# Optimization experiments

Hardware: AMD Instinct MI355X
Metric: run time of the kernel (lower is better)

## Reference

```python
import math
import jax, jax.numpy as jnp
import numpy as np

CLUSTER_RATIO1 = 0.0625
CLUSTER_RATIO2 = 0.35
K_LAYER1 = 8
K_LAYER2 = 3


def _dpc_knn(x, cluster_num, k, key):
    """Density-peak clustering with KNN density. x: [B,N,C] -> idx_cluster [B,N]."""
    B, N, C = x.shape
    sq = jnp.sum(x * x, axis=-1)  # [B,N]
    d2 = sq[:, :, None] + sq[:, None, :] - 2.0 * jnp.einsum('bnc,bmc->bnm', x, x)
    dist = jnp.sqrt(jnp.maximum(d2, 0.0)) / jnp.sqrt(jnp.asarray(C, x.dtype))  # cdist / C**0.5
    # k nearest (smallest) distances
    neg_dn, _ = jax.lax.top_k(-dist, k)
    dist_nearest = -neg_dn  # [B,N,k]
    density = jnp.exp(-jnp.mean(dist_nearest ** 2, axis=-1))
    density = density + jax.random.uniform(key, density.shape, dtype=density.dtype) * 1e-6
    mask = (density[:, None, :] > density[:, :, None]).astype(x.dtype)  # [B,N,N]
    dist_max = jnp.max(dist.reshape(B, -1), axis=-1)[:, None, None]
    parent_dist = jnp.min(dist * mask + dist_max * (1.0 - mask), axis=-1)  # [B,N]
    score = parent_dist * density
    _, index_down = jax.lax.top_k(score, cluster_num)  # [B,cluster_num] cluster centers
    # assign each token to nearest center
    dm = jnp.take_along_axis(dist, index_down[:, :, None], axis=1)  # [B,cluster_num,N]
    idx_cluster = jnp.argmin(dm, axis=1)  # [B,N]
    bidx = jnp.arange(B)[:, None]
    idx_cluster = idx_cluster.at[bidx, index_down].set(
        jnp.broadcast_to(jnp.arange(cluster_num)[None, :], index_down.shape))
    return idx_cluster


def _merge_tokens(x, idx_cluster, cluster_num):
    """Weighted (uniform) scatter-mean of tokens into clusters. x: [B,N,C]."""
    B, N, C = x.shape
    flat = (idx_cluster + jnp.arange(B)[:, None] * cluster_num).reshape(-1)  # [B*N]
    ones = jnp.ones((B * N,), x.dtype)
    all_w = jax.ops.segment_sum(ones, flat, num_segments=B * cluster_num) + 1e-6
    norm_w = 1.0 / all_w[flat]  # token_weight == 1
    merged = jax.ops.segment_sum(x.reshape(B * N, C) * norm_w[:, None], flat,
                                 num_segments=B * cluster_num)
    return merged.reshape(B, cluster_num, C)


def _group(meta1, meta2, idx_cluster2, score_w, score_b):
    """Reorder [meta2[v]; members of cluster v from meta1] per cluster, scaled by modulation."""
    T, K1, C = meta1.shape
    K2 = meta2.shape[1]
    modu = jax.nn.softmax(meta2.mean(axis=2) @ score_w.T + score_b, axis=-1)  # [T,K2]
    # composite sort key: (cluster_id, 0 for meta2 center, 1+i for meta1 member i) -> stable grouping
    cid = jnp.concatenate([jnp.broadcast_to(jnp.arange(K2)[None, :], (T, K2)),
                           idx_cluster2], axis=1)  # [T,K2+K1]
    pos = jnp.concatenate([jnp.zeros((T, K2), jnp.int32),
                           jnp.broadcast_to(jnp.arange(1, K1 + 1, dtype=jnp.int32)[None, :], (T, K1))],
                          axis=1)
    sort_key = cid * (K1 + 2) + pos
    order = jnp.argsort(sort_key, axis=1)  # stable; keys are unique anyway
    tokens = jnp.concatenate([meta2, meta1], axis=1)  # [T,K2+K1,C]
    sorted_tokens = jnp.take_along_axis(tokens, order[:, :, None], axis=1)
    sorted_cid = jnp.take_along_axis(cid, order, axis=1)
    scale = jnp.take_along_axis(modu, sorted_cid, axis=1)  # [T,K2+K1]
    return sorted_tokens * scale[:, :, None]


def setup_inputs() -> dict:
    key = jax.random.key(0)
    k1, k2, k3 = jax.random.split(key, 3)
    T, N, C = 128, 256, 1408
    vis_embed = jax.random.normal(k1, (T, N, C), dtype=jnp.float32)
    score_w = jax.random.normal(k2, (6, 6), dtype=jnp.float32) * 0.1
    score_b = jax.random.normal(k3, (6,), dtype=jnp.float32) * 0.1
    return {"vis_embed": vis_embed, "score_w": score_w, "score_b": score_b}


def reference(vis_embed, score_w, score_b):
    T, N, C = vis_embed.shape
    cn1 = max(math.ceil(N * CLUSTER_RATIO1), 1)      # 16
    cn2 = max(math.ceil(cn1 * CLUSTER_RATIO2), 1)    # 6
    nk = jax.random.split(jax.random.key(42), 2)
    idx1 = _dpc_knn(vis_embed, cn1, K_LAYER1, nk[0])
    meta1 = _merge_tokens(vis_embed, idx1, cn1)       # [T,16,C]
    idx2 = _dpc_knn(meta1, cn2, K_LAYER2, nk[1])
    meta2 = _merge_tokens(meta1, idx2, cn2)           # [T,6,C]
    return _group(meta1, meta2, idx2, score_w, score_b)  # [T,22,C]
```

## Files before the change

### kernel.cpp

```cpp
#include <hip/hip_runtime.h>
#include <math.h>

#define T_BATCH 128
#define N_TOK   256
#define C_DIM   1408
#define CN1     16
#define KNN1    8
#define CN2     6
#define KNN2    3
#define NOUT    22
#define LS      44

typedef __attribute__((ext_vector_type(4))) short sh4;
typedef __attribute__((ext_vector_type(8))) short sh8;
typedef __attribute__((ext_vector_type(4))) float f32x4;

union frag_u { sh4 h[2]; sh8 v; };

__device__ inline sh8 ld_frag(const short* p) {
    frag_u u;
    u.h[0] = *(const sh4*)p;
    u.h[1] = *(const sh4*)(p + 4);
    return u.v;
}

__device__ inline void split2(float v0, float v1, unsigned& hip, unsigned& lop) {
    unsigned u0 = __float_as_uint(v0);
    unsigned u1 = __float_as_uint(v1);
    hip = (u0 >> 16) | (u1 & 0xFFFF0000u);
    float l0 = v0 - __uint_as_float(u0 & 0xFFFF0000u);
    float l1 = v1 - __uint_as_float(u1 & 0xFFFF0000u);
    unsigned w0 = __float_as_uint(l0);
    unsigned w1 = __float_as_uint(l1);
    w0 = w0 + 0x7FFFu + ((w0 >> 16) & 1u);
    w1 = w1 + 0x7FFFu + ((w1 >> 16) & 1u);
    lop = (w0 >> 16) | (w1 & 0xFFFF0000u);
}

#define INS8(m, v) {                                   \
    float _x = (v);                                    \
    _Pragma("unroll")                                  \
    for (int _q = 0; _q < 8; _q++) {                   \
        float _lo = fminf(m[_q], _x);                  \
        _x = fmaxf(m[_q], _x);                         \
        m[_q] = _lo;                                   \
    }                                                  \
}

__global__ __launch_bounds__(256, 4) void gemm_dist_sym(const float* __restrict__ x,
                                                        float* __restrict__ dist) {
    const int id = blockIdx.x;
    const int r  = id & 7;
    const int q8 = id >> 3;
    const int p  = q8 % 10;
    const int tt = q8 / 10;
    const int t  = tt * 8 + r;
    const int bi = (p < 4) ? 0 : (p < 7) ? 1 : (p < 9) ? 2 : 3;
    const int bj = (p < 4) ? p : (p < 7) ? p - 3 : (p < 9) ? p - 5 : 3;
    const int i0 = bi * 64, j0 = bj * 64;
    const bool diag = (bi == bj);
    const float* X = x + (size_t)t * N_TOK * C_DIM;

    __shared__ short Ahi[64 * LS], Alo[64 * LS], Bhi[64 * LS], Blo[64 * LS];
    __shared__ float nred[512];
    __shared__ float snA[64], snB[64];

    const int tid  = threadIdx.x;
    const int wave = tid >> 6;
    const int lane = tid & 63;
    const int qr   = wave >> 1;
    const int qc   = wave & 1;
    const int srow = tid >> 2;
    const int sq   = tid & 3;
    const int fr   = lane & 15;
    const int fq   = lane >> 4;

    const short* BhiS = diag ? Ahi : Bhi;
    const short* BloS = diag ? Alo : Blo;

    f32x4 acc[2][2];
#pragma unroll
    for (int a = 0; a < 2; a++)
#pragma unroll
        for (int b = 0; b < 2; b++) acc[a][b] = (f32x4){0.f, 0.f, 0.f, 0.f};

    const float* Arow = X + (size_t)(i0 + srow) * C_DIM + sq * 8;
    const float* Brow = X + (size_t)(j0 + srow) * C_DIM + sq * 8;
    float nA = 0.f, nB = 0.f;

    float4 a0 = *(const float4*)(Arow + 0);
    float4 a1 = *(const float4*)(Arow + 4);
    float4 b0 = {0.f, 0.f, 0.f, 0.f}, b1 = {0.f, 0.f, 0.f, 0.f};
    if (!diag) {
        b0 = *(const float4*)(Brow + 0);
        b1 = *(const float4*)(Brow + 4);
    }

    for (int k0 = 0; k0 < C_DIM; k0 += 32) {
        float av[8], bv[8];
        av[0] = a0.x; av[1] = a0.y; av[2] = a0.z; av[3] = a0.w;
        av[4] = a1.x; av[5] = a1.y; av[6] = a1.z; av[7] = a1.w;
#pragma unroll
        for (int e = 0; e < 8; e++) nA += av[e] * av[e];
        unsigned ah[4], al[4], bh[4], bl[4];
#pragma unroll
        for (int q = 0; q < 4; q++) split2(av[2 * q], av[2 * q + 1], ah[q], al[q]);
        if (!diag) {
            bv[0] = b0.x; bv[1] = b0.y; bv[2] = b0.z; bv[3] = b0.w;
            bv[4] = b1.x; bv[5] = b1.y; bv[6] = b1.z; bv[7] = b1.w;
#pragma unroll
            for (int e = 0; e < 8; e++) nB += bv[e] * bv[e];
#pragma unroll
            for (int q = 0; q < 4; q++) split2(bv[2 * q], bv[2 * q + 1], bh[q], bl[q]);
        }
        __syncthreads();
        {
            unsigned* AH = (unsigned*)&Ahi[srow * LS + sq * 8];
            unsigned* AL = (unsigned*)&Alo[srow * LS + sq * 8];
#pragma unroll
            for (int q = 0; q < 4; q++) { AH[q] = ah[q]; AL[q] = al[q]; }
            if (!diag) {
                unsigned* BH = (unsigned*)&Bhi[srow * LS + sq * 8];
                unsigned* BL = (unsigned*)&Blo[srow * LS + sq * 8];
#pragma unroll
                for (int q = 0; q < 4; q++) { BH[q] = bh[q]; BL[q] = bl[q]; }
            }
        }
        __syncthreads();

        const int k1 = k0 + 32;
        if (k1 < C_DIM) {
            a0 = *(const float4*)(Arow + k1);
            a1 = *(const float4*)(Arow + k1 + 4);
            if (!diag) {
                b0 = *(const float4*)(Brow + k1);
                b1 = *(const float4*)(Brow + k1 + 4);
            }
        }

        sh8 fAh[2], fAl[2], fBh[2], fBl[2];
#pragma unroll
        for (int mt = 0; mt < 2; mt++) {
            int ro = (qr * 32 + mt * 16 + fr) * LS + fq * 8;
            fAh[mt] = ld_frag(&Ahi[ro]);
            fAl[mt] = ld_frag(&Alo[ro]);
            int co = (qc * 32 + mt * 16 + fr) * LS + fq * 8;
            fBh[mt] = ld_frag(&BhiS[co]);
            fBl[mt] = ld_frag(&BloS[co]);
        }
#pragma unroll
        for (int mt = 0; mt < 2; mt++)
#pragma unroll
            for (int nt = 0; nt < 2; nt++) {
                acc[mt][nt] = __builtin_amdgcn_mfma_f32_16x16x32_bf16(fAh[mt], fBh[nt], acc[mt][nt], 0, 0, 0);
                acc[mt][nt] = __builtin_amdgcn_mfma_f32_16x16x32_bf16(fAh[mt], fBl[nt], acc[mt][nt], 0, 0, 0);
                acc[mt][nt] = __builtin_amdgcn_mfma_f32_16x16x32_bf16(fAl[mt], fBh[nt], acc[mt][nt], 0, 0, 0);
            }
    }

    nred[tid] = nA;
    nred[256 + tid] = diag ? nA : nB;
    __syncthreads();
    if (tid < 64) {
        snA[tid] = nred[4 * tid] + nred[4 * tid + 1] + nred[4 * tid + 2] + nred[4 * tid + 3];
        snB[tid] = nred[256 + 4 * tid] + nred[256 + 4 * tid + 1]
                 + nred[256 + 4 * tid + 2] + nred[256 + 4 * tid + 3];
    }
    __syncthreads();

    const float inv_sqrtC = 1.0f / sqrtf((float)C_DIM);
    float* Dt = dist + (size_t)t * N_TOK * N_TOK;
#pragma unroll
    for (int mt = 0; mt < 2; mt++)
#pragma unroll
        for (int nt = 0; nt < 2; nt++) {
            int jl = qc * 32 + nt * 16 + fr;
            int jg = j0 + jl;
            float sqj = snB[jl];
            int il0 = qr * 32 + mt * 16 + fq * 4;
            float vv[4];
#pragma unroll
            for (int rr = 0; rr < 4; rr++) {
                int ig = i0 + il0 + rr;
                float d2 = snA[il0 + rr] + sqj - 2.0f * acc[mt][nt][rr];
                float v = (ig == jg) ? 0.0f : sqrtf(fmaxf(d2, 0.0f)) * inv_sqrtC;
                Dt[(size_t)ig * N_TOK + jg] = v;
                vv[rr] = v;
            }
            if (!diag) {
                float4 o; o.x = vv[0]; o.y = vv[1]; o.z = vv[2]; o.w = vv[3];
                *(float4*)&Dt[(size_t)jg * N_TOK + i0 + il0] = o;
            }
        }
}

__global__ __launch_bounds__(1024) void dpc1_fused(const float* __restrict__ dist,
                                                   int* __restrict__ memb,
                                                   int* __restrict__ cntg,
                                                   int* __restrict__ offg) {
    const int t    = blockIdx.x;
    const int tid  = threadIdx.x;
    const int col  = tid & 255;
    const int h    = tid >> 8;
    const int lane = tid & 63;
    const int wid  = tid >> 6;
    const float* D = dist + (size_t)t * N_TOK * N_TOK;

    __shared__ float dens_s[N_TOK];
    __shared__ float lists[KNN1][1024];
    __shared__ float red[1024];
    __shared__ float rmax16[16];
    __shared__ unsigned long long wred[16];
    __shared__ int centers[CN1];
    __shared__ int bks[N_TOK];
    __shared__ int cnt_s[CN1], off_s[CN1];

    float c0[8], c1[8];
#pragma unroll
    for (int q = 0; q < 8; q++) { c0[q] = 3.4e38f; c1[q] = 3.4e38f; }
    float mx = 0.f;
    const float* base = D + (size_t)(h * 64) * N_TOK + col;
    for (int jj = 0; jj < 64; jj += 2) {
        float d0 = base[(size_t)(jj + 0) * N_TOK];
        float d1 = base[(size_t)(jj + 1) * N_TOK];
        mx = fmaxf(mx, fmaxf(d0, d1));
        INS8(c0, d0); INS8(c1, d1);
    }
#pragma unroll
    for (int q = 0; q < 8; q++) { INS8(c0, c1[q]); }
#pragma unroll
    for (int q = 0; q < 8; q++) lists[q][tid] = c0[q];
#pragma unroll
    for (int off = 32; off > 0; off >>= 1) mx = fmaxf(mx, __shfl_xor(mx, off));
    if (lane == 0) rmax16[wid] = mx;
    __syncthreads();
    float dmax = rmax16[0];
#pragma unroll
    for (int w = 1; w < 16; w++) dmax = fmaxf(dmax, rmax16[w]);

    if (h == 0) {
#pragma unroll
        for (int s = 1; s < 4; s++)
#pragma unroll
            for (int q = 0; q < 8; q++) { float v = lists[q][col + s * 256]; INS8(c0, v); }
        float s2 = 0.f;
#pragma unroll
        for (int q = 0; q < 8; q++) s2 += c0[q] * c0[q];
        dens_s[col] = expf(-s2 / (float)KNN1);
    }
    __syncthreads();
    const float dens = dens_s[col];

    float p0 = dmax, p1 = dmax;
    const float* dsh = dens_s + h * 64;
    for (int jj = 0; jj < 64; jj += 2) {
        float d0 = base[(size_t)(jj + 0) * N_TOK];
        float d1 = base[(size_t)(jj + 1) * N_TOK];
        p0 = (dsh[jj + 0] > dens) ? fminf(p0, d0) : p0;
        p1 = (dsh[jj + 1] > dens) ? fminf(p1, d1) : p1;
    }
    red[tid] = fminf(p0, p1);
    __syncthreads();
    float score = 0.f;
    if (h == 0)
        score = fminf(fminf(red[col], red[col + 256]),
                      fminf(red[col + 512], red[col + 768])) * dens;

    unsigned long long key = 0;
    if (h == 0)
        key = ((unsigned long long)__float_as_uint(score) << 32) | (unsigned)(65535 - col);
    for (int k = 0; k < CN1; k++) {
        unsigned long long mm = key;
#pragma unroll
        for (int off = 32; off > 0; off >>= 1) {
            unsigned long long o = __shfl_xor(mm, off);
            mm = (o > mm) ? o : mm;
        }
        if (lane == 0) wred[wid] = mm;
        __syncthreads();
        unsigned long long b = wred[0];
#pragma unroll
        for (int w = 1; w < 16; w++) b = (wred[w] > b) ? wred[w] : b;
        int idx = 65535 - (int)(b & 0xFFFFull);
        if (tid == 0) centers[k] = idx;
        if (tid == idx) key = 0;
        __syncthreads();
    }

    int bk = 0;
    if (h == 0) {
        float bd = 3.4e38f;
#pragma unroll
        for (int k = 0; k < CN1; k++) {
            float d = D[(size_t)centers[k] * N_TOK + col];
            if (d < bd) { bd = d; bk = k; }
        }
#pragma unroll
        for (int k = 0; k < CN1; k++) if (col == centers[k]) bk = k;
        bks[col] = bk;
    }
    __syncthreads();
    if (tid < CN1) {
        int c = 0;
        for (int j = 0; j < N_TOK; j++) c += (bks[j] == tid);
        cnt_s[tid] = c;
    }
    __syncthreads();
    if (tid == 0) {
        int o = 0;
        for (int q = 0; q < CN1; q++) { off_s[q] = o; o += cnt_s[q]; }
    }
    __syncthreads();
    if (h == 0) {
        int rank = 0;
        for (int j = 0; j < col; j++) rank += (bks[j] == bk);
        memb[t * N_TOK + off_s[bk] + rank] = col;
    }
    if (tid < CN1) {
        cntg[t * CN1 + tid] = cnt_s[tid];
        offg[t * CN1 + tid] = off_s[tid];
    }
}

__global__ __launch_bounds__(256) void merge1_kernel(const float* __restrict__ x,
                                                     const int* __restrict__ memb,
                                                     const int* __restrict__ cntg,
                                                     const int* __restrict__ offg,
                                                     float* __restrict__ meta1) {
    const int q   = blockIdx.x;
    const int t   = blockIdx.y;
    const int tid = threadIdx.x;
    const int n    = cntg[t * CN1 + q];
    const int base = t * N_TOK + offg[t * CN1 + q];
    const int c0 = tid, c1 = tid + 256;
    const bool act1 = (c1 < C_DIM / 4);
    const float4* xb = (const float4*)(x + (size_t)t * N_TOK * C_DIM);
    const int stride4 = C_DIM / 4;

    float4 s0 = {0.f, 0.f, 0.f, 0.f};
    float4 s1 = {0.f, 0.f, 0.f, 0.f};
    int m = 0;
    for (; m + 4 <= n; m += 4) {
        int r0 = memb[base + m + 0];
        int r1 = memb[base + m + 1];
        int r2 = memb[base + m + 2];
        int r3 = memb[base + m + 3];
        float4 a0 = xb[(size_t)r0 * stride4 + c0];
        float4 a1 = xb[(size_t)r1 * stride4 + c0];
        float4 a2 = xb[(size_t)r2 * stride4 + c0];
        float4 a3 = xb[(size_t)r3 * stride4 + c0];
        s0.x += a0.x; s0.y += a0.y; s0.z += a0.z; s0.w += a0.w;
        s0.x += a1.x; s0.y += a1.y; s0.z += a1.z; s0.w += a1.w;
        s0.x += a2.x; s0.y += a2.y; s0.z += a2.z; s0.w += a2.w;
        s0.x += a3.x; s0.y += a3.y; s0.z += a3.z; s0.w += a3.w;
        if (act1) {
            float4 b0 = xb[(size_t)r0 * stride4 + c1];
            float4 b1 = xb[(size_t)r1 * stride4 + c1];
            float4 b2 = xb[(size_t)r2 * stride4 + c1];
            float4 b3 = xb[(size_t)r3 * stride4 + c1];
            s1.x += b0.x; s1.y += b0.y; s1.z += b0.z; s1.w += b0.w;
            s1.x += b1.x; s1.y += b1.y; s1.z += b1.z; s1.w += b1.w;
            s1.x += b2.x; s1.y += b2.y; s1.z += b2.z; s1.w += b2.w;
            s1.x += b3.x; s1.y += b3.y; s1.z += b3.z; s1.w += b3.w;
        }
    }
    for (; m < n; m++) {
        int r0 = memb[base + m];
        float4 a0 = xb[(size_t)r0 * stride4 + c0];
        s0.x += a0.x; s0.y += a0.y; s0.z += a0.z; s0.w += a0.w;
        if (act1) {
            float4 b0 = xb[(size_t)r0 * stride4 + c1];
            s1.x += b0.x; s1.y += b0.y; s1.z += b0.z; s1.w += b0.w;
        }
    }
    float w = 1.0f / ((float)n + 1e-6f);
    float4* mr = (float4*)(meta1 + ((size_t)t * CN1 + q) * C_DIM);
    float4 o0; o0.x = s0.x * w; o0.y = s0.y * w; o0.z = s0.z * w; o0.w = s0.w * w;
    mr[c0] = o0;
    if (act1) {
        float4 o1; o1.x = s1.x * w; o1.y = s1.y * w; o1.z = s1.z * w; o1.w = s1.w * w;
        mr[c1] = o1;
    }
}

__global__ __launch_bounds__(1024) void layer2_kernel(const float* __restrict__ meta1,
                                                      const float* __restrict__ score_w,
                                                      const float* __restrict__ score_b,
                                                      float* __restrict__ out) {
    const int t   = blockIdx.x;
    const int tid = threadIdx.x;
    const float* M = meta1 + (size_t)t * CN1 * C_DIM;

    __shared__ float buf[CN1][132];
    __shared__ float d2s[CN1][CN1];
    __shared__ float m2[CN2][C_DIM];
    __shared__ float dens[CN1], scor[CN1], nrm[CN1], rmx[CN1];
    __shared__ int   centers[CN2], idx2s[CN1], cnt2[CN2];
    __shared__ float modu[CN2], msum[CN2];
    __shared__ int   srcRow[NOUT], cidArr[NOUT];
    __shared__ float dmax_sh;

    const int ti = (tid < 256) ? (tid >> 4) : 0;
    const int tj = tid & 15;

    float acc = 0.f;
    for (int c0 = 0; c0 < C_DIM; c0 += 128) {
        for (int e = tid; e < CN1 * 128; e += 1024) {
            int r = e >> 7, c = e & 127;
            buf[r][c] = M[(size_t)r * C_DIM + c0 + c];
        }
        __syncthreads();
        if (tid < 256) {
#pragma unroll
            for (int cc = 0; cc < 128; cc += 4) {
                float4 a = *(const float4*)&buf[ti][cc];
                float4 b = *(const float4*)&buf[tj][cc];
                acc += a.x * b.x + a.y * b.y + a.z * b.z + a.w * b.w;
            }
        }
        __syncthreads();
    }
    if (tid < 256 && ti == tj) nrm[ti] = acc;
    __syncthreads();

    const float inv_sqrtC = 1.0f / sqrtf((float)C_DIM);
    if (tid < 256) {
        float d2 = nrm[ti] + nrm[tj] - 2.f * acc;
        d2s[ti][tj] = sqrtf(fmaxf(d2, 0.f)) * inv_sqrtC;
    }
    __syncthreads();

    if (tid < CN1) {
        float m0 = 3.4e38f, m1 = 3.4e38f, m2v = 3.4e38f, mx = 0.f;
        for (int j = 0; j < CN1; j++) {
            float d = d2s[tid][j];
            mx = fmaxf(mx, d);
            if (d < m2v) {
                m2v = d;
                if (m2v < m1) { float tmp = m2v; m2v = m1; m1 = tmp; }
                if (m1 < m0)  { float tmp = m1;  m1 = m0;  m0 = tmp; }
            }
        }
        dens[tid] = expf(-(m0 * m0 + m1 * m1 + m2v * m2v) / (float)KNN2);
        rmx[tid] = mx;
    }
    __syncthreads();
    if (tid == 0) {
        float g = 0.f;
        for (int j = 0; j < CN1; j++) g = fmaxf(g, rmx[j]);
        dmax_sh = g;
    }
    __syncthreads();

    if (tid < CN1) {
        float di = dens[tid];
        float pd = dmax_sh;
        for (int j = 0; j < CN1; j++)
            if (dens[j] > di) pd = fminf(pd, d2s[tid][j]);
        scor[tid] = pd * di;
    }
    __syncthreads();

    if (tid == 0) {
        for (int k = 0; k < CN2; k++) {
            float best = -3.4e38f; int bi = 0;
            for (int j = 0; j < CN1; j++)
                if (scor[j] > best) { best = scor[j]; bi = j; }
            centers[k] = bi;
            scor[bi] = -3.4e38f;
        }
    }
    __syncthreads();

    if (tid < CN1) {
        float bd = 3.4e38f; int bk = 0;
#pragma unroll
        for (int k = 0; k < CN2; k++) {
            float d = d2s[centers[k]][tid];
            if (d < bd) { bd = d; bk = k; }
        }
#pragma unroll
        for (int k = 0; k < CN2; k++) if (tid == centers[k]) bk = k;
        idx2s[tid] = bk;
    }
    __syncthreads();

    if (tid == 0) {
        for (int v = 0; v < CN2; v++) cnt2[v] = 0;
        for (int i = 0; i < CN1; i++) cnt2[idx2s[i]]++;
        int slot = 0;
        for (int v = 0; v < CN2; v++) {
            srcRow[slot] = CN1 + v; cidArr[slot] = v; slot++;
            for (int i = 0; i < CN1; i++)
                if (idx2s[i] == v) { srcRow[slot] = i; cidArr[slot] = v; slot++; }
        }
        for (int v = 0; v < CN2; v++) msum[v] = 0.f;
    }
    __syncthreads();

    float ls[CN2] = {0.f, 0.f, 0.f, 0.f, 0.f, 0.f};
    for (int ch = tid; ch < C_DIM; ch += 1024) {
        float a6[CN2] = {0.f, 0.f, 0.f, 0.f, 0.f, 0.f};
        for (int r = 0; r < CN1; r++) {
            float v = M[(size_t)r * C_DIM + ch];
            int c = idx2s[r];
#pragma unroll
            for (int q = 0; q < CN2; q++) a6[q] += (c == q) ? v : 0.f;
        }
#pragma unroll
        for (int q = 0; q < CN2; q++) {
            float mv = a6[q] / ((float)cnt2[q] + 1e-6f);
            m2[q][ch] = mv;
            ls[q] += mv;
        }
    }
#pragma unroll
    for (int q = 0; q < CN2; q++) atomicAdd(&msum[q], ls[q]);
    __syncthreads();

    if (tid == 0) {
        float mean[CN2], lg[CN2];
        for (int v = 0; v < CN2; v++) mean[v] = msum[v] / (float)C_DIM;
        float mxl = -3.4e38f;
        for (int u = 0; u < CN2; u++) {
            float s = score_b[u];
            for (int v = 0; v < CN2; v++) s += mean[v] * score_w[u * CN2 + v];
            lg[u] = s;
            mxl = fmaxf(mxl, s);
        }
        float den = 0.f;
        for (int u = 0; u < CN2; u++) { lg[u] = expf(lg[u] - mxl); den += lg[u]; }
        for (int u = 0; u < CN2; u++) modu[u] = lg[u] / den;
    }
    __syncthreads();

    float* ob = out + (size_t)t * NOUT * C_DIM;
    for (int ch = tid; ch < C_DIM; ch += 1024) {
#pragma unroll
        for (int s = 0; s < NOUT; s++) {
            int r = srcRow[s];
            float v = (r < CN1) ? M[(size_t)r * C_DIM + ch] : m2[r - CN1][ch];
            ob[(size_t)s * C_DIM + ch] = v * modu[cidArr[s]];
        }
    }
}

extern "C" void kernel_launch(void* const* d_in, const int* in_sizes, int n_in,
                              void* d_out, int out_size, void* d_ws, size_t ws_size,
                              hipStream_t stream) {
    const float* x  = (const float*)d_in[0];
    const float* sw = (const float*)d_in[1];
    const float* sb = (const float*)d_in[2];
    float* out = (float*)d_out;

    float* ws     = (float*)d_ws;
    float* dist   = ws;
    float* meta1  = dist + (size_t)T_BATCH * N_TOK * N_TOK;
    int*   memb   = (int*)(meta1 + (size_t)T_BATCH * CN1 * C_DIM);
    int*   cntg   = memb + (size_t)T_BATCH * N_TOK;
    int*   offg   = cntg + T_BATCH * CN1;

    gemm_dist_sym<<<1280, 256, 0, stream>>>(x, dist);
    dpc1_fused<<<T_BATCH, 1024, 0, stream>>>(dist, memb, cntg, offg);
    merge1_kernel<<<dim3(CN1, T_BATCH), 256, 0, stream>>>(x, memb, cntg, offg, meta1);
    layer2_kernel<<<T_BATCH, 1024, 0, stream>>>(meta1, sw, sb, out);
}
```

Before: 421.8 us.

## Replace symmetric 64x64 tile Gram kernel with per-batch half-matrix blocks

The distance GEMM now runs one 512-thread block per half of each batch's 256x256 Gram matrix. Each block loads all 256 rows of a 32-wide K slice into shared memory once and computes a 128x256 output with 4x4 MFMA tiles per wave. Before, 1280 blocks each read two 64-row panels and used symmetry to mirror-write off-diagonal tiles. The change cuts redundant global reads and the split/convert work per element, but it drops the symmetry saving, so the lower triangle is recomputed. It also shrinks the grid to 256 blocks and raises per-thread accumulator register pressure.

```diff
diff --git a/kernel.cpp b/kernel.cpp
--- a/kernel.cpp
+++ b/kernel.cpp
@@ -9,7 +9,7 @@
 #define CN2     6
 #define KNN2    3
 #define NOUT    22
-#define LS      44
+#define LS2     36
 
 typedef __attribute__((ext_vector_type(4))) short sh4;
 typedef __attribute__((ext_vector_type(8))) short sh8;
@@ -47,149 +47,119 @@
     }                                                  \
 }
 
-__global__ __launch_bounds__(256, 4) void gemm_dist_sym(const float* __restrict__ x,
-                                                        float* __restrict__ dist) {
+__global__ __launch_bounds__(512, 2) void gemm_dist_half(const float* __restrict__ x,
+                                                         float* __restrict__ dist) {
     const int id = blockIdx.x;
     const int r  = id & 7;
-    const int q8 = id >> 3;
-    const int p  = q8 % 10;
-    const int tt = q8 / 10;
-    const int t  = tt * 8 + r;
-    const int bi = (p < 4) ? 0 : (p < 7) ? 1 : (p < 9) ? 2 : 3;
-    const int bj = (p < 4) ? p : (p < 7) ? p - 3 : (p < 9) ? p - 5 : 3;
-    const int i0 = bi * 64, j0 = bj * 64;
-    const bool diag = (bi == bj);
+    const int u  = id >> 3;
+    const int h  = u & 1;
+    const int t  = (u >> 1) * 8 + r;
     const float* X = x + (size_t)t * N_TOK * C_DIM;
 
-    __shared__ short Ahi[64 * LS], Alo[64 * LS], Bhi[64 * LS], Blo[64 * LS];
+    __shared__ short Phi[N_TOK * LS2];
+    __shared__ short Plo[N_TOK * LS2];
     __shared__ float nred[512];
-    __shared__ float snA[64], snB[64];
+    __shared__ float sn[N_TOK];
 
     const int tid  = threadIdx.x;
     const int wave = tid >> 6;
     const int lane = tid & 63;
-    const int qr   = wave >> 1;
-    const int qc   = wave & 1;
-    const int srow = tid >> 2;
-    const int sq   = tid & 3;
+    const int wr   = wave >> 2;
+    const int wc   = wave & 3;
+    const int srow = tid >> 1;
+    const int sq   = tid & 1;
     const int fr   = lane & 15;
     const int fq   = lane >> 4;
 
-    const short* BhiS = diag ? Ahi : Bhi;
-    const short* BloS = diag ? Alo : Blo;
-
-    f32x4 acc[2][2];
-#pragma unroll
-    for (int a = 0; a < 2; a++)
-#pragma unroll
-        for (int b = 0; b < 2; b++) acc[a][b] = (f32x4){0.f, 0.f, 0.f, 0.f};
-
-    const float* Arow = X + (size_t)(i0 + srow) * C_DIM + sq * 8;
-    const float* Brow = X + (size_t)(j0 + srow) * C_DIM + sq * 8;
-    float nA = 0.f, nB = 0.f;
-
-    float4 a0 = *(const float4*)(Arow + 0);
-    float4 a1 = *(const float4*)(Arow + 4);
-    float4 b0 = {0.f, 0.f, 0.f, 0.f}, b1 = {0.f, 0.f, 0.f, 0.f};
-    if (!diag) {
-        b0 = *(const float4*)(Brow + 0);
-        b1 = *(const float4*)(Brow + 4);
-    }
+    f32x4 acc[4][4];
+#pragma unroll
+    for (int a = 0; a < 4; a++)
+#pragma unroll
+        for (int b = 0; b < 4; b++) acc[a][b] = (f32x4){0.f, 0.f, 0.f, 0.f};
+
+    const float* Row = X + (size_t)srow * C_DIM + sq * 16;
+    float nA = 0.f;
+
+    float4 a0 = *(const float4*)(Row + 0);
+    float4 a1 = *(const float4*)(Row + 4);
+    float4 a2 = *(const float4*)(Row + 8);
+    float4 a3 = *(const float4*)(Row + 12);
 
     for (int k0 = 0; k0 < C_DIM; k0 += 32) {
-        float av[8], bv[8];
-        av[0] = a0.x; av[1] = a0.y; av[2] = a0.z; av[3] = a0.w;
-        av[4] = a1.x; av[5] = a1.y; av[6] = a1.z; av[7] = a1.w;
-#pragma unroll
-        for (int e = 0; e < 8; e++) nA += av[e] * av[e];
-        unsigned ah[4], al[4], bh[4], bl[4];
-#pragma unroll
-        for (int q = 0; q < 4; q++) split2(av[2 * q], av[2 * q + 1], ah[q], al[q]);
-        if (!diag) {
-            bv[0] = b0.x; bv[1] = b0.y; bv[2] = b0.z; bv[3] = b0.w;
-            bv[4] = b1.x; bv[5] = b1.y; bv[6] = b1.z; bv[7] = b1.w;
-#pragma unroll
-            for (int e = 0; e < 8; e++) nB += bv[e] * bv[e];
-#pragma unroll
-            for (int q = 0; q < 4; q++) split2(bv[2 * q], bv[2 * q + 1], bh[q], bl[q]);
-        }
+        float av[16];
+        av[0]  = a0.x; av[1]  = a0.y; av[2]  = a0.z; av[3]  = a0.w;
+        av[4]  = a1.x; av[5]  = a1.y; av[6]  = a1.z; av[7]  = a1.w;
+        av[8]  = a2.x; av[9]  = a2.y; av[10] = a2.z; av[11] = a2.w;
+        av[12] = a3.x; av[13] = a3.y; av[14] = a3.z; av[15] = a3.w;
+#pragma unroll
+        for (int e = 0; e < 16; e++) nA += av[e] * av[e];
+        unsigned hh[8], ll[8];
+#pragma unroll
+        for (int q = 0; q < 8; q++) split2(av[2 * q], av[2 * q + 1], hh[q], ll[q]);
+
         __syncthreads();
         {
-            unsigned* AH = (unsigned*)&Ahi[srow * LS + sq * 8];
-            unsigned* AL = (unsigned*)&Alo[srow * LS + sq * 8];
-#pragma unroll
-            for (int q = 0; q < 4; q++) { AH[q] = ah[q]; AL[q] = al[q]; }
-            if (!diag) {
-                unsigned* BH = (unsigned*)&Bhi[srow * LS + sq * 8];
-                unsigned* BL = (unsigned*)&Blo[srow * LS + sq * 8];
-#pragma unroll
-                for (int q = 0; q < 4; q++) { BH[q] = bh[q]; BL[q] = bl[q]; }
+            uint2* WH = (uint2*)&Phi[srow * LS2 + sq * 16];
+            uint2* WL = (uint2*)&Plo[srow * LS2 + sq * 16];
+#pragma unroll
+            for (int q = 0; q < 4; q++) {
+                uint2 vh; vh.x = hh[2 * q]; vh.y = hh[2 * q + 1];
+                uint2 vl; vl.x = ll[2 * q]; vl.y = ll[2 * q + 1];
+                WH[q] = vh;
+                WL[q] = vl;
             }
         }
         __syncthreads();
 
         const int k1 = k0 + 32;
         if (k1 < C_DIM) {
-            a0 = *(const float4*)(Arow + k1);
-            a1 = *(const float4*)(Arow + k1 + 4);
-            if (!diag) {
-                b0 = *(const float4*)(Brow + k1);
-                b1 = *(const float4*)(Brow + k1 + 4);
+            a0 = *(const float4*)(Row + k1);
+            a1 = *(const float4*)(Row + k1 + 4);
+            a2 = *(const float4*)(Row + k1 + 8);
+            a3 = *(const float4*)(Row + k1 + 12);
+        }
+
+        sh8 fAh[4], fAl[4];
+#pragma unroll
+        for (int mt = 0; mt < 4; mt++) {
+            int ao = (h * 128 + wr * 64 + mt * 16 + fr) * LS2 + fq * 8;
+            fAh[mt] = ld_frag(&Phi[ao]);
+            fAl[mt] = ld_frag(&Plo[ao]);
+        }
+#pragma unroll
+        for (int nt = 0; nt < 4; nt++) {
+            int bo = (wc * 64 + nt * 16 + fr) * LS2 + fq * 8;
+            sh8 fBh = ld_frag(&Phi[bo]);
+            sh8 fBl = ld_frag(&Plo[bo]);
+#pragma unroll
+            for (int mt = 0; mt < 4; mt++) {
+                acc[mt][nt] = __builtin_amdgcn_mfma_f32_16x16x32_bf16(fAh[mt], fBh, acc[mt][nt], 0, 0, 0);
+                acc[mt][nt] = __builtin_amdgcn_mfma_f32_16x16x32_bf16(fAh[mt], fBl, acc[mt][nt], 0, 0, 0);
+                acc[mt][nt] = __builtin_amdgcn_mfma_f32_16x16x32_bf16(fAl[mt], fBh, acc[mt][nt], 0, 0, 0);
             }
         }
-
-        sh8 fAh[2], fAl[2], fBh[2], fBl[2];
-#pragma unroll
-        for (int mt = 0; mt < 2; mt++) {
-            int ro = (qr * 32 + mt * 16 + fr) * LS + fq * 8;
-            fAh[mt] = ld_frag(&Ahi[ro]);
-            fAl[mt] = ld_frag(&Alo[ro]);
-            int co = (qc * 32 + mt * 16 + fr) * LS + fq * 8;
-            fBh[mt] = ld_frag(&BhiS[co]);
-            fBl[mt] = ld_frag(&BloS[co]);
-        }
-#pragma unroll
-        for (int mt = 0; mt < 2; mt++)
-#pragma unroll
-            for (int nt = 0; nt < 2; nt++) {
-                acc[mt][nt] = __builtin_amdgcn_mfma_f32_16x16x32_bf16(fAh[mt], fBh[nt], acc[mt][nt], 0, 0, 0);
-                acc[mt][nt] = __builtin_amdgcn_mfma_f32_16x16x32_bf16(fAh[mt], fBl[nt], acc[mt][nt], 0, 0, 0);
-                acc[mt][nt] = __builtin_amdgcn_mfma_f32_16x16x32_bf16(fAl[mt], fBh[nt], acc[mt][nt], 0, 0, 0);
-            }
     }
 
     nred[tid] = nA;
-    nred[256 + tid] = diag ? nA : nB;
-    __syncthreads();
-    if (tid < 64) {
-        snA[tid] = nred[4 * tid] + nred[4 * tid + 1] + nred[4 * tid + 2] + nred[4 * tid + 3];
-        snB[tid] = nred[256 + 4 * tid] + nred[256 + 4 * tid + 1]
-                 + nred[256 + 4 * tid + 2] + nred[256 + 4 * tid + 3];
-    }
+    __syncthreads();
+    if (tid < N_TOK) sn[tid] = nred[2 * tid] + nred[2 * tid + 1];
     __syncthreads();
 
     const float inv_sqrtC = 1.0f / sqrtf((float)C_DIM);
     float* Dt = dist + (size_t)t * N_TOK * N_TOK;
 #pragma unroll
-    for (int mt = 0; mt < 2; mt++)
-#pragma unroll
-        for (int nt = 0; nt < 2; nt++) {
-            int jl = qc * 32 + nt * 16 + fr;
-            int jg = j0 + jl;
-            float sqj = snB[jl];
-            int il0 = qr * 32 + mt * 16 + fq * 4;
-            float vv[4];
+    for (int mt = 0; mt < 4; mt++)
+#pragma unroll
+        for (int nt = 0; nt < 4; nt++) {
+            int jg = wc * 64 + nt * 16 + fr;
+            float sqj = sn[jg];
+            int i0 = h * 128 + wr * 64 + mt * 16 + fq * 4;
 #pragma unroll
             for (int rr = 0; rr < 4; rr++) {
-                int ig = i0 + il0 + rr;
-                float d2 = snA[il0 + rr] + sqj - 2.0f * acc[mt][nt][rr];
+                int ig = i0 + rr;
+                float d2 = sn[ig] + sqj - 2.0f * acc[mt][nt][rr];
                 float v = (ig == jg) ? 0.0f : sqrtf(fmaxf(d2, 0.0f)) * inv_sqrtC;
                 Dt[(size_t)ig * N_TOK + jg] = v;
-                vv[rr] = v;
-            }
-            if (!diag) {
-                float4 o; o.x = vv[0]; o.y = vv[1]; o.z = vv[2]; o.w = vv[3];
-                *(float4*)&Dt[(size_t)jg * N_TOK + i0 + il0] = o;
             }
         }
 }
@@ -560,7 +530,7 @@
     int*   cntg   = memb + (size_t)T_BATCH * N_TOK;
     int*   offg   = cntg + T_BATCH * CN1;
 
-    gemm_dist_sym<<<1280, 256, 0, stream>>>(x, dist);
+    gemm_dist_half<<<256, 512, 0, stream>>>(x, dist);
     dpc1_fused<<<T_BATCH, 1024, 0, stream>>>(dist, memb, cntg, offg);
     merge1_kernel<<<dim3(CN1, T_BATCH), 256, 0, stream>>>(x, memb, cntg, offg, meta1);
     layer2_kernel<<<T_BATCH, 1024, 0, stream>>>(meta1, sw, sb, out);
```

After: 435.1 us. 3.2% more time.
